# Performance work log

Hardware: AMD Instinct MI355X
Metric: run time of the kernel (lower is better)

Reference implementation:

```python
import jax, jax.numpy as jnp
import numpy as np

N_ATOMS = 16384
N_BLOCKS = 4096
K = 3          # top-k nearest context atoms (min(3, n_ctx) in original; n_ctx >> 3 here)
EPS_W = 1e-8   # inverse-distance weight epsilon (matches original)
EPS_D = 1e-12  # tiny epsilon inside sqrt for numerical safety of the distance


def setup_inputs() -> dict:
    key = jax.random.key(0)
    k1, k2, k3, k4, k5 = jax.random.split(key, 5)
    # coordinates spread out like real molecular coords (Angstrom-ish scale)
    X = jax.random.normal(k1, (N_ATOMS, 3), dtype=jnp.float32) * 10.0
    base_noise = jax.random.normal(k2, (N_ATOMS, 3), dtype=jnp.float32)      # randn_like(X)
    centroid_noise = jax.random.normal(k3, (N_ATOMS, 3), dtype=jnp.float32)  # per-atom randn(3)
    block_ids = jnp.sort(jax.random.randint(k4, (N_ATOMS,), 0, N_BLOCKS)).astype(jnp.int32)
    generate_mask = jax.random.randint(k5, (N_BLOCKS,), 0, 2).astype(bool)
    return {
        "X": X,
        "base_noise": base_noise,
        "centroid_noise": centroid_noise,
        "block_ids": block_ids,
        "generate_mask": generate_mask,
    }


def reference(X, base_noise, centroid_noise, block_ids, generate_mask):
    """Vectorized sample_chemical_prior: for every generated atom, find the 3
    nearest CONTEXT atoms, take an inverse-distance-weighted centroid, and add
    0.5 * gaussian noise. Non-generated atoms keep base_noise (randn_like)."""
    n = X.shape[0]
    gen_atoms = generate_mask[block_ids]           # [N] atoms being generated
    ctx = ~gen_atoms                               # [N] context atoms

    # pairwise squared distances via ||a||^2 + ||b||^2 - 2 a.b  -> [N, N]
    xn = jnp.sum(X * X, axis=-1)
    sq = xn[:, None] + xn[None, :] - 2.0 * (X @ X.T)
    d = jnp.sqrt(jnp.maximum(sq, 0.0) + EPS_D)

    # only context atoms are valid neighbor candidates; exclude self for safety
    not_self = ~jnp.eye(n, dtype=bool)
    d = jnp.where(ctx[None, :] & not_self, d, jnp.inf)

    # k nearest context atoms per row (smallest distances)
    neg_dk, idx = jax.lax.top_k(-d, K)             # [N, K]
    dk = -neg_dk

    # inverse-distance weights, normalized (matches original)
    w = 1.0 / (dk + EPS_W)
    w = w / jnp.sum(w, axis=-1, keepdims=True)

    coords = X[idx]                                # [N, K, 3] gather neighbor coords
    centroid = jnp.sum(coords * w[..., None], axis=1)  # [N, 3]

    x0 = jnp.where(gen_atoms[:, None], centroid + 0.5 * centroid_noise, base_noise)
    return x0
```

## Files before the change

kernel.cpp:

```cpp
#include <hip/hip_runtime.h>
#include <cstdint>

#define N_ATOMS 16384
#define NBLK 64
#define NTHR 256
#define G 24
#define NCELLS 13824
#define NCELLS_PAD 14336
#define CPT 14
#define BOX_LO -48.0f
#define INV_CELL 0.25f
#define SINIT 3.0e38f

#define OFF_COUNTS 0
#define OFF_ACELL 256
#define OFF_START 33280
#define OFF_GENIDX 90880
#define OFF_CTX4 156672

__device__ __forceinline__ int cell1(float x) {
    int c = (int)floorf((x - BOX_LO) * INV_CELL);
    return min(max(c, 0), G - 1);
}

__device__ __forceinline__ void ins3(float v, int vi,
                                     float& s1, float& s2, float& s3,
                                     int& i1, int& i2, int& i3)
{
    const bool b1 = v < s1, b2 = v < s2, b3 = v < s3;
    s3 = b2 ? s2 : (b3 ? v : s3);   i3 = b2 ? i2 : (b3 ? vi : i3);
    s2 = b1 ? s1 : (b2 ? v : s2);   i2 = b1 ? i1 : (b2 ? vi : i2);
    s1 = b1 ? v : s1;               i1 = b1 ? vi : i1;
}

__global__ __launch_bounds__(NTHR)
void k1_classify(const float* __restrict__ X,
                 const int* __restrict__ block_ids,
                 const unsigned int* __restrict__ mask,
                 const float* __restrict__ base_noise,
                 float* __restrict__ out,
                 unsigned short* __restrict__ acell)
{
    __shared__ int sflag;
    const int t = threadIdx.x;

    if (t == 0) sflag = 0;
    __syncthreads();
    if (mask[t] > 1u) sflag = 1;
    __syncthreads();
    const bool is_u8 = (sflag != 0);
    const unsigned char* m8 = (const unsigned char*)mask;

    const int i = blockIdx.x * NTHR + t;
    const int bid = block_ids[i];
    const bool g = is_u8 ? (m8[bid] != 0) : (mask[bid] != 0u);

    out[3 * i + 0] = base_noise[3 * i + 0];
    out[3 * i + 1] = base_noise[3 * i + 1];
    out[3 * i + 2] = base_noise[3 * i + 2];

    unsigned short c = 0xFFFFu;
    if (!g) {
        const float x = X[3 * i], y = X[3 * i + 1], z = X[3 * i + 2];
        c = (unsigned short)((cell1(z) * G + cell1(y)) * G + cell1(x));
    }
    acell[i] = c;
}

__global__ __launch_bounds__(1024)
void k2_sortscatter(const float* __restrict__ X,
                    const unsigned short* __restrict__ acell,
                    int* __restrict__ cell_start,
                    int* __restrict__ counts,
                    int* __restrict__ genidx,
                    float4* __restrict__ ctx4s)
{
    __shared__ int hist[NCELLS_PAD];
    __shared__ int wsum[16], wexc[16];
    __shared__ int gcnt;
    const int t = threadIdx.x;
    const int wave = t >> 6, lane = t & 63;

    #pragma unroll
    for (int k = 0; k < CPT; ++k) hist[t * CPT + k] = 0;
    if (t == 0) gcnt = 0;
    __syncthreads();

    #pragma unroll
    for (int it = 0; it < N_ATOMS / 1024; ++it) {
        const unsigned short c = acell[it * 1024 + t];
        if (c != 0xFFFFu) atomicAdd(&hist[c], 1);
    }
    __syncthreads();

    int loc[CPT]; int sum = 0;
    #pragma unroll
    for (int k = 0; k < CPT; ++k) {
        const int v = hist[t * CPT + k];
        loc[k] = sum; sum += v;
    }
    int v = sum;
    #pragma unroll
    for (int d = 1; d < 64; d <<= 1) { const int u = __shfl_up(v, d); if (lane >= d) v += u; }
    if (lane == 63) wsum[wave] = v;
    __syncthreads();
    if (t < 16) {
        int v2 = wsum[t];
        const int orig = v2;
        #pragma unroll
        for (int d = 1; d < 16; d <<= 1) { const int u = __shfl_up(v2, d); if (t >= d) v2 += u; }
        wexc[t] = v2 - orig;
    }
    __syncthreads();
    const int base = wexc[wave] + (v - sum);
    #pragma unroll
    for (int k = 0; k < CPT; ++k) {
        const int st = base + loc[k];
        cell_start[t * CPT + k] = st;
        hist[t * CPT + k] = st;
    }
    if (t == 1023) cell_start[NCELLS_PAD] = base + sum;
    __syncthreads();

    #pragma unroll
    for (int it = 0; it < N_ATOMS / 1024; ++it) {
        const int i = it * 1024 + t;
        const unsigned short c = acell[i];
        if (c != 0xFFFFu) {
            const int p = atomicAdd(&hist[c], 1);
            const float x = X[3 * i], y = X[3 * i + 1], z = X[3 * i + 2];
            float xn = x * x; xn += y * y; xn += z * z;
            ctx4s[p] = make_float4(x, y, z, xn);
        } else {
            genidx[atomicAdd(&gcnt, 1)] = i;
        }
    }
    __syncthreads();
    if (t == 0) { counts[1] = gcnt; counts[0] = N_ATOMS - gcnt; }
}

__global__ __launch_bounds__(NTHR)
void k4_search(const float* __restrict__ X,
               const float* __restrict__ cnoise,
               const int* __restrict__ counts,
               const int* __restrict__ cell_start,
               const float4* __restrict__ ctx4s,
               const int* __restrict__ genidx,
               float* __restrict__ out)
{
    const int n_gen = counts[1];
    const int wave = threadIdx.x >> 6, lane = threadIdx.x & 63;
    if ((int)blockIdx.x * 4 >= n_gen) return;
    const int slot = (int)blockIdx.x * 4 + wave;
    if (slot >= n_gen) return;

    const int ai = genidx[slot];
    const float qx = X[3 * ai], qy = X[3 * ai + 1], qz = X[3 * ai + 2];
    float xnq = qx * qx; xnq += qy * qy; xnq += qz * qz;
    const int cqx = cell1(qx), cqy = cell1(qy), cqz = cell1(qz);

    float s1 = SINIT, s2 = SINIT, s3 = SINIT;
    int i1 = 0, i2 = 0, i3 = 0;

    {
        int st = 0, cnt = 0;
        if (lane < 9) {
            const int dy = lane % 3 - 1, dz = lane / 3 - 1;
            const int cy = cqy + dy, cz = cqz + dz;
            if ((unsigned)cy < G && (unsigned)cz < G) {
                const int xlo = max(cqx - 1, 0), xhi = min(cqx + 1, G - 1);
                const int c0 = (cz * G + cy) * G + xlo;
                st = cell_start[c0];
                cnt = cell_start[c0 + (xhi - xlo + 1)] - st;
            }
        }
        int stv[9], base[10];
        base[0] = 0;
        #pragma unroll
        for (int k = 0; k < 9; ++k) {
            stv[k] = __builtin_amdgcn_readlane(st, k);
            base[k + 1] = base[k] + __builtin_amdgcn_readlane(cnt, k);
        }
        const int T = base[9];
        const int nro = (T + 63) >> 6;
        if (nro > 0) {
            auto calcP = [&](int j) -> int {
                const int jc = min(j, T - 1);
                int p = stv[0] + jc;
                #pragma unroll
                for (int k = 1; k < 9; ++k)
                    p = (jc >= base[k]) ? stv[k] + (jc - base[k]) : p;
                return p;
            };
            int p0 = calcP(lane);
            float4 cc0 = ctx4s[p0];
            for (int ro = 0; ro < nro; ++ro) {
                int p1 = p0; float4 cc1 = cc0;
                if (ro + 1 < nro) { p1 = calcP((ro + 1) * 64 + lane); cc1 = ctx4s[p1]; }
                if (ro * 64 + lane < T) {
                    const float dot = qx * cc0.x + qy * cc0.y + qz * cc0.z;
                    const float sq = (xnq + cc0.w) - 2.0f * dot;
                    ins3(sq, p0, s1, s2, s3, i1, i2, i3);
                }
                p0 = p1; cc0 = cc1;
            }
        }
    }

    const int cb = __popcll(__ballot(s1 + 0.01f < 16.0f))
                 + __popcll(__ballot(s2 + 0.01f < 16.0f))
                 + __popcll(__ballot(s3 + 0.01f < 16.0f));

    if (cb < 3) {
        s1 = SINIT; s2 = SINIT; s3 = SINIT;
        i1 = 0; i2 = 0; i3 = 0;
        const int n_ctx = counts[0];
        for (int base = 0; base < n_ctx; base += 512) {
            float4 cv0, cv1, cv2, cv3, cv4, cv5, cv6, cv7;
            const int pa0 = min(base + 0 * 64 + lane, n_ctx - 1);
            const int pa1 = min(base + 1 * 64 + lane, n_ctx - 1);
            const int pa2 = min(base + 2 * 64 + lane, n_ctx - 1);
            const int pa3 = min(base + 3 * 64 + lane, n_ctx - 1);
            const int pa4 = min(base + 4 * 64 + lane, n_ctx - 1);
            const int pa5 = min(base + 5 * 64 + lane, n_ctx - 1);
            const int pa6 = min(base + 6 * 64 + lane, n_ctx - 1);
            const int pa7 = min(base + 7 * 64 + lane, n_ctx - 1);
            cv0 = ctx4s[pa0]; cv1 = ctx4s[pa1]; cv2 = ctx4s[pa2]; cv3 = ctx4s[pa3];
            cv4 = ctx4s[pa4]; cv5 = ctx4s[pa5]; cv6 = ctx4s[pa6]; cv7 = ctx4s[pa7];
            #define TAIL_INS(K, CV, PA) \
                if (base + (K) * 64 + lane < n_ctx) { \
                    const float dot = qx * (CV).x + qy * (CV).y + qz * (CV).z; \
                    const float sq = (xnq + (CV).w) - 2.0f * dot; \
                    ins3(sq, (PA), s1, s2, s3, i1, i2, i3); \
                }
            TAIL_INS(0, cv0, pa0) TAIL_INS(1, cv1, pa1)
            TAIL_INS(2, cv2, pa2) TAIL_INS(3, cv3, pa3)
            TAIL_INS(4, cv4, pa4) TAIL_INS(5, cv5, pa5)
            TAIL_INS(6, cv6, pa6) TAIL_INS(7, cv7, pa7)
            #undef TAIL_INS
        }
    }

    #pragma unroll
    for (int m = 1; m < 64; m <<= 1) {
        const float a = __shfl_xor(s1, m); const int ja = __shfl_xor(i1, m);
        const float b = __shfl_xor(s2, m); const int jb = __shfl_xor(i2, m);
        const float c = __shfl_xor(s3, m); const int jc = __shfl_xor(i3, m);
        ins3(a, ja, s1, s2, s3, i1, i2, i3);
        ins3(b, jb, s1, s2, s3, i1, i2, i3);
        ins3(c, jc, s1, s2, s3, i1, i2, i3);
    }

    if (lane == 0) {
        const float d1 = sqrtf(fmaxf(s1, 0.0f) + 1e-12f);
        const float d2 = sqrtf(fmaxf(s2, 0.0f) + 1e-12f);
        const float d3 = sqrtf(fmaxf(s3, 0.0f) + 1e-12f);
        float w1 = 1.0f / (d1 + 1e-8f);
        float w2 = 1.0f / (d2 + 1e-8f);
        float w3 = 1.0f / (d3 + 1e-8f);
        float wsum = w1 + w2;
        wsum += w3;
        w1 /= wsum; w2 /= wsum; w3 /= wsum;
        const float4 c1 = ctx4s[i1];
        const float4 c2 = ctx4s[i2];
        const float4 c3 = ctx4s[i3];
        float cxo = w1 * c1.x + w2 * c2.x; cxo += w3 * c3.x;
        float cyo = w1 * c1.y + w2 * c2.y; cyo += w3 * c3.y;
        float czo = w1 * c1.z + w2 * c2.z; czo += w3 * c3.z;
        out[3 * ai + 0] = cxo + 0.5f * cnoise[3 * ai + 0];
        out[3 * ai + 1] = cyo + 0.5f * cnoise[3 * ai + 1];
        out[3 * ai + 2] = czo + 0.5f * cnoise[3 * ai + 2];
    }
}

extern "C" void kernel_launch(void* const* d_in, const int* in_sizes, int n_in,
                              void* d_out, int out_size, void* d_ws, size_t ws_size,
                              hipStream_t stream) {
    const float* X          = (const float*)d_in[0];
    const float* base_noise = (const float*)d_in[1];
    const float* cnoise     = (const float*)d_in[2];
    const int*   block_ids  = (const int*)d_in[3];
    const unsigned int* gmask = (const unsigned int*)d_in[4];
    float* out = (float*)d_out;

    char* ws = (char*)d_ws;
    int*    counts     = (int*)(ws + OFF_COUNTS);
    unsigned short* acell = (unsigned short*)(ws + OFF_ACELL);
    int*    cell_start = (int*)(ws + OFF_START);
    int*    genidx     = (int*)(ws + OFF_GENIDX);
    float4* ctx4s      = (float4*)(ws + OFF_CTX4);

    k1_classify<<<NBLK, NTHR, 0, stream>>>(X, block_ids, gmask, base_noise,
                                           out, acell);
    k2_sortscatter<<<1, 1024, 0, stream>>>(X, acell, cell_start, counts,
                                           genidx, ctx4s);
    k4_search<<<N_ATOMS / 4, NTHR, 0, stream>>>(X, cnoise, counts, cell_start,
                                                ctx4s, genidx, out);
}
```

Measured before the change: 54.49 us.

## Add intermediate shell search, atomic-free genidx scatter, and DPP wave merge

Generated-atom indices are now placed by adding per-chunk bins for generated atoms to the existing histogram, which removes the serialized shared-memory atomic counter. In the search kernel, a query that does not converge within radius 16 now scans an extra shell of cells (radius 2 minus radius 1) before falling back to a brute-force scan of all context atoms. The final top-3 wave reduction replaces shfl_xor with DPP and swizzle permutes to lower cross-lane latency. Correctness of the DPP patterns and of the shell enumeration is the main risk.

```diff
diff --git a/kernel.cpp b/kernel.cpp
--- a/kernel.cpp
+++ b/kernel.cpp
@@ -77,19 +77,19 @@
 {
     __shared__ int hist[NCELLS_PAD];
     __shared__ int wsum[16], wexc[16];
-    __shared__ int gcnt;
     const int t = threadIdx.x;
     const int wave = t >> 6, lane = t & 63;
 
     #pragma unroll
     for (int k = 0; k < CPT; ++k) hist[t * CPT + k] = 0;
-    if (t == 0) gcnt = 0;
     __syncthreads();
 
     #pragma unroll
     for (int it = 0; it < N_ATOMS / 1024; ++it) {
-        const unsigned short c = acell[it * 1024 + t];
-        if (c != 0xFFFFu) atomicAdd(&hist[c], 1);
+        const int i = it * 1024 + t;
+        const unsigned short c = acell[i];
+        const int bin = (c == 0xFFFFu) ? (NCELLS + ((i >> 8) & 63)) : (int)c;
+        atomicAdd(&hist[bin], 1);
     }
     __syncthreads();
 
@@ -122,22 +122,32 @@
     if (t == 1023) cell_start[NCELLS_PAD] = base + sum;
     __syncthreads();
 
+    const int nctx = hist[NCELLS];
+    __syncthreads();
+
     #pragma unroll
     for (int it = 0; it < N_ATOMS / 1024; ++it) {
         const int i = it * 1024 + t;
         const unsigned short c = acell[i];
+        const int bin = (c == 0xFFFFu) ? (NCELLS + ((i >> 8) & 63)) : (int)c;
+        const int p = atomicAdd(&hist[bin], 1);
         if (c != 0xFFFFu) {
-            const int p = atomicAdd(&hist[c], 1);
             const float x = X[3 * i], y = X[3 * i + 1], z = X[3 * i + 2];
             float xn = x * x; xn += y * y; xn += z * z;
             ctx4s[p] = make_float4(x, y, z, xn);
         } else {
-            genidx[atomicAdd(&gcnt, 1)] = i;
-        }
-    }
-    __syncthreads();
-    if (t == 0) { counts[1] = gcnt; counts[0] = N_ATOMS - gcnt; }
-}
+            genidx[p - nctx] = i;
+        }
+    }
+    if (t == 0) { counts[0] = nctx; counts[1] = N_ATOMS - nctx; }
+}
+
+#define P_X1(v)  __builtin_amdgcn_update_dpp(v, v, 0xB1, 0xF, 0xF, false)
+#define P_X2(v)  __builtin_amdgcn_update_dpp(v, v, 0x4E, 0xF, 0xF, false)
+#define P_R4(v)  __builtin_amdgcn_update_dpp(v, v, 0x124, 0xF, 0xF, false)
+#define P_R8(v)  __builtin_amdgcn_update_dpp(v, v, 0x128, 0xF, 0xF, false)
+#define P_S16(v) __builtin_amdgcn_ds_swizzle(v, 0x401F)
+#define P_X32(v) __shfl_xor(v, 32)
 
 __global__ __launch_bounds__(NTHR)
 void k4_search(const float* __restrict__ X,
@@ -207,49 +217,133 @@
         }
     }
 
-    const int cb = __popcll(__ballot(s1 + 0.01f < 16.0f))
-                 + __popcll(__ballot(s2 + 0.01f < 16.0f))
-                 + __popcll(__ballot(s3 + 0.01f < 16.0f));
-
-    if (cb < 3) {
-        s1 = SINIT; s2 = SINIT; s3 = SINIT;
-        i1 = 0; i2 = 0; i3 = 0;
-        const int n_ctx = counts[0];
-        for (int base = 0; base < n_ctx; base += 512) {
-            float4 cv0, cv1, cv2, cv3, cv4, cv5, cv6, cv7;
-            const int pa0 = min(base + 0 * 64 + lane, n_ctx - 1);
-            const int pa1 = min(base + 1 * 64 + lane, n_ctx - 1);
-            const int pa2 = min(base + 2 * 64 + lane, n_ctx - 1);
-            const int pa3 = min(base + 3 * 64 + lane, n_ctx - 1);
-            const int pa4 = min(base + 4 * 64 + lane, n_ctx - 1);
-            const int pa5 = min(base + 5 * 64 + lane, n_ctx - 1);
-            const int pa6 = min(base + 6 * 64 + lane, n_ctx - 1);
-            const int pa7 = min(base + 7 * 64 + lane, n_ctx - 1);
-            cv0 = ctx4s[pa0]; cv1 = ctx4s[pa1]; cv2 = ctx4s[pa2]; cv3 = ctx4s[pa3];
-            cv4 = ctx4s[pa4]; cv5 = ctx4s[pa5]; cv6 = ctx4s[pa6]; cv7 = ctx4s[pa7];
-            #define TAIL_INS(K, CV, PA) \
-                if (base + (K) * 64 + lane < n_ctx) { \
-                    const float dot = qx * (CV).x + qy * (CV).y + qz * (CV).z; \
-                    const float sq = (xnq + (CV).w) - 2.0f * dot; \
-                    ins3(sq, (PA), s1, s2, s3, i1, i2, i3); \
-                }
-            TAIL_INS(0, cv0, pa0) TAIL_INS(1, cv1, pa1)
-            TAIL_INS(2, cv2, pa2) TAIL_INS(3, cv3, pa3)
-            TAIL_INS(4, cv4, pa4) TAIL_INS(5, cv5, pa5)
-            TAIL_INS(6, cv6, pa6) TAIL_INS(7, cv7, pa7)
-            #undef TAIL_INS
-        }
-    }
-
-    #pragma unroll
-    for (int m = 1; m < 64; m <<= 1) {
-        const float a = __shfl_xor(s1, m); const int ja = __shfl_xor(i1, m);
-        const float b = __shfl_xor(s2, m); const int jb = __shfl_xor(i2, m);
-        const float c = __shfl_xor(s3, m); const int jc = __shfl_xor(i3, m);
-        ins3(a, ja, s1, s2, s3, i1, i2, i3);
-        ins3(b, jb, s1, s2, s3, i1, i2, i3);
-        ins3(c, jc, s1, s2, s3, i1, i2, i3);
-    }
+    auto converged = [&](float bnd) -> bool {
+        const int c = __popcll(__ballot(s1 + 0.01f < bnd))
+                    + __popcll(__ballot(s2 + 0.01f < bnd))
+                    + __popcll(__ballot(s3 + 0.01f < bnd));
+        return c >= 3;
+    };
+
+    bool done = converged(16.0f);
+
+    if (!done) {
+        {
+            const int P = 1, R = 2;
+            const int B = 2 * R + 1;
+            const int RP = R - P;
+            const int PP = 2 * P + 1;
+            const int A = 2 * RP * B;
+            const int C = PP * 2 * RP;
+            const int NS = A + C + 2 * PP * PP;
+            int st = 0, cnt = 0;
+            if (lane < NS) {
+                const int u = lane;
+                int dy, dz, xlo, xhi;
+                if (u < A) {
+                    const int q = u / B, rdy = u - q * B;
+                    dz = (q < RP) ? (-R + q) : (P + 1 + (q - RP));
+                    dy = rdy - R;
+                    xlo = cqx - R; xhi = cqx + R;
+                } else if (u < A + C) {
+                    const int v2 = u - A, W = 2 * RP;
+                    const int q = v2 / W, w = v2 - q * W;
+                    dz = -P + q;
+                    dy = (w < RP) ? (-R + w) : (P + 1 + (w - RP));
+                    xlo = cqx - R; xhi = cqx + R;
+                } else {
+                    const int v2 = u - A - C;
+                    const int side = v2 & 1, v3 = v2 >> 1;
+                    dy = v3 % PP - P; dz = v3 / PP - P;
+                    if (side) { xlo = cqx + P + 1; xhi = cqx + R; }
+                    else      { xlo = cqx - R;     xhi = cqx - P - 1; }
+                }
+                const int cy = cqy + dy, cz = cqz + dz;
+                if ((unsigned)cy < G && (unsigned)cz < G) {
+                    xlo = max(xlo, 0); xhi = min(xhi, G - 1);
+                    if (xlo <= xhi) {
+                        const int c0 = (cz * G + cy) * G + xlo;
+                        st = cell_start[c0];
+                        cnt = cell_start[c0 + (xhi - xlo + 1)] - st;
+                    }
+                }
+            }
+            int pre = cnt;
+            #pragma unroll
+            for (int d = 1; d < 64; d <<= 1) {
+                const int u = __shfl_up(pre, d);
+                if (lane >= d) pre += u;
+            }
+            const int T = __shfl(pre, 63);
+            const int ebase = pre - cnt;
+            const int pk = st - ebase;
+            const int iters = (T + 63) >> 6;
+            for (int it = 0; it < iters; ++it) {
+                const int j = it * 64 + lane;
+                const int jc = min(j, T - 1);
+                int L = 0;
+                #pragma unroll
+                for (int stp = 32; stp >= 1; stp >>= 1) {
+                    const int cand = L + stp;
+                    const int bv = __shfl(ebase, cand);
+                    if (bv <= jc) L = cand;
+                }
+                const int p = __shfl(pk, L) + jc;
+                const float4 cc = ctx4s[p];
+                if (j < T) {
+                    const float dot = qx * cc.x + qy * cc.y + qz * cc.z;
+                    const float sq = (xnq + cc.w) - 2.0f * dot;
+                    ins3(sq, p, s1, s2, s3, i1, i2, i3);
+                }
+            }
+        }
+        done = converged(64.0f);
+
+        if (!done) {
+            s1 = SINIT; s2 = SINIT; s3 = SINIT;
+            i1 = 0; i2 = 0; i3 = 0;
+            const int n_ctx = counts[0];
+            for (int base = 0; base < n_ctx; base += 512) {
+                const int pa0 = min(base + 0 * 64 + lane, n_ctx - 1);
+                const int pa1 = min(base + 1 * 64 + lane, n_ctx - 1);
+                const int pa2 = min(base + 2 * 64 + lane, n_ctx - 1);
+                const int pa3 = min(base + 3 * 64 + lane, n_ctx - 1);
+                const int pa4 = min(base + 4 * 64 + lane, n_ctx - 1);
+                const int pa5 = min(base + 5 * 64 + lane, n_ctx - 1);
+                const int pa6 = min(base + 6 * 64 + lane, n_ctx - 1);
+                const int pa7 = min(base + 7 * 64 + lane, n_ctx - 1);
+                const float4 cv0 = ctx4s[pa0], cv1 = ctx4s[pa1];
+                const float4 cv2 = ctx4s[pa2], cv3 = ctx4s[pa3];
+                const float4 cv4 = ctx4s[pa4], cv5 = ctx4s[pa5];
+                const float4 cv6 = ctx4s[pa6], cv7 = ctx4s[pa7];
+                #define TAIL_INS(K, CV, PA) \
+                    if (base + (K) * 64 + lane < n_ctx) { \
+                        const float dot = qx * (CV).x + qy * (CV).y + qz * (CV).z; \
+                        const float sq = (xnq + (CV).w) - 2.0f * dot; \
+                        ins3(sq, (PA), s1, s2, s3, i1, i2, i3); \
+                    }
+                TAIL_INS(0, cv0, pa0) TAIL_INS(1, cv1, pa1)
+                TAIL_INS(2, cv2, pa2) TAIL_INS(3, cv3, pa3)
+                TAIL_INS(4, cv4, pa4) TAIL_INS(5, cv5, pa5)
+                TAIL_INS(6, cv6, pa6) TAIL_INS(7, cv7, pa7)
+                #undef TAIL_INS
+            }
+        }
+    }
+
+    #define MERGE_STEP(PERM) { \
+        const float a = __int_as_float(PERM(__float_as_int(s1))); const int ja = PERM(i1); \
+        const float b = __int_as_float(PERM(__float_as_int(s2))); const int jb = PERM(i2); \
+        const float c = __int_as_float(PERM(__float_as_int(s3))); const int jc = PERM(i3); \
+        ins3(a, ja, s1, s2, s3, i1, i2, i3); \
+        ins3(b, jb, s1, s2, s3, i1, i2, i3); \
+        ins3(c, jc, s1, s2, s3, i1, i2, i3); }
+    MERGE_STEP(P_X1)
+    MERGE_STEP(P_X2)
+    MERGE_STEP(P_R4)
+    MERGE_STEP(P_R8)
+    MERGE_STEP(P_S16)
+    MERGE_STEP(P_X32)
+    #undef MERGE_STEP
 
     if (lane == 0) {
         const float d1 = sqrtf(fmaxf(s1, 0.0f) + 1e-12f);
```

Result: faster. 53.20 us (-2.4%).
